# Performance work log

Hardware: AMD Instinct MI355X
Metric: run time of the kernel (lower is better)

The kernel has to match this reference:

```python
import jax, jax.numpy as jnp
import numpy as np

D_MODEL = 1024
N_HEADS = 16
D_HEAD = D_MODEL // N_HEADS


def setup_inputs() -> dict:
    key = jax.random.key(0)
    ks = jax.random.split(key, 11)
    B, S = 2, 2048
    s_in = 1.0 / np.sqrt(D_MODEL)
    return {
        "query": jax.random.normal(ks[0], (B, S, D_MODEL), jnp.float32),
        "key": jax.random.normal(ks[1], (B, S, D_MODEL), jnp.float32),
        "value": jax.random.normal(ks[2], (B, S, D_MODEL), jnp.float32),
        "Wq_w": jax.random.normal(ks[3], (D_MODEL, D_MODEL), jnp.float32) * s_in,
        "Wq_b": jax.random.normal(ks[4], (D_MODEL,), jnp.float32) * 0.01,
        "Wk_w": jax.random.normal(ks[5], (D_HEAD, D_MODEL), jnp.float32) * s_in,
        "Wk_b": jax.random.normal(ks[6], (D_HEAD,), jnp.float32) * 0.01,
        "Wv_w": jax.random.normal(ks[7], (D_HEAD, D_MODEL), jnp.float32) * s_in,
        "Wv_b": jax.random.normal(ks[8], (D_HEAD,), jnp.float32) * 0.01,
        "Wo_w": jax.random.normal(ks[9], (D_MODEL, D_MODEL), jnp.float32) * s_in,
        "Wo_b": jax.random.normal(ks[10], (D_MODEL,), jnp.float32) * 0.01,
    }


def reference(query, key, value, Wq_w, Wq_b, Wk_w, Wk_b, Wv_w, Wv_b, Wo_w, Wo_b):
    B, S, _ = query.shape
    # Q: per-head projection [B, H, S, dh]; K/V: single shared head [B, S, dh]
    Q = (query @ Wq_w.T + Wq_b).reshape(B, S, N_HEADS, D_HEAD).transpose(0, 2, 1, 3)
    K = key @ Wk_w.T + Wk_b      # [B, S, dh], shared across heads (MQA)
    V = value @ Wv_w.T + Wv_b    # [B, S, dh]
    scale = 1.0 / np.sqrt(D_HEAD).astype(np.float32)
    scores = jnp.einsum('bhqd,bkd->bhqk', Q, K) * scale  # [B, H, S, S]
    attn = jax.nn.softmax(scores, axis=-1)
    ctx = jnp.einsum('bhqk,bkd->bhqd', attn, V)           # [B, H, S, dh]
    ctx = ctx.transpose(0, 2, 1, 3).reshape(B, S, D_MODEL)
    out = ctx @ Wo_w.T + Wo_b
    return out, attn
```

## Files before the change

### kernel.cpp

```cpp
#include <hip/hip_runtime.h>
#include <hip/hip_bf16.h>
#include <math.h>

#define D_MODEL 1024
#define N_HEADS 16
#define D_HEAD 64
#define S_ 2048

typedef __attribute__((ext_vector_type(8))) short short8;
typedef __attribute__((ext_vector_type(4))) float f32x4;
typedef __attribute__((ext_vector_type(16))) float f32x16;

static __device__ inline short f2bf(float f) {
    union { __hip_bfloat16 h; short s; } u;
    u.h = __float2bfloat16(f);
    return u.s;
}

static __device__ inline f32x4 mfma16(short8 a, short8 b, f32x4 c) {
    return __builtin_amdgcn_mfma_f32_16x16x32_bf16(a, b, c, 0, 0, 0);
}
static __device__ inline f32x16 mfma32(short8 a, short8 b, f32x16 c) {
    return __builtin_amdgcn_mfma_f32_32x32x16_bf16(a, b, c, 0, 0, 0);
}
static __device__ inline f32x16 zero16() {
    f32x16 z;
#pragma unroll
    for (int i = 0; i < 16; i++) z[i] = 0.f;
    return z;
}

static __device__ inline void load_lds16(const void* g, void* l) {
    __builtin_amdgcn_global_load_lds(
        (const __attribute__((address_space(1))) unsigned int*)g,
        (__attribute__((address_space(3))) unsigned int*)l, 16, 0, 0);
}

__global__ __launch_bounds__(256)
void cvt_all(const float* __restrict__ q, const float* __restrict__ k,
             const float* __restrict__ v, const float* __restrict__ wq,
             const float* __restrict__ wk, const float* __restrict__ wv,
             const float* __restrict__ wo,
             short* dq, short* dk, short* dv, short* dwq, short* dwk,
             short* dwv, short* dwo) {
    size_t c = (size_t)blockIdx.x * 256 + threadIdx.x;
    const float* s; short* d; size_t off;
    if (c < 524288)        { s = q;  d = dq;  off = c; }
    else if (c < 1048576)  { s = k;  d = dk;  off = c - 524288; }
    else if (c < 1572864)  { s = v;  d = dv;  off = c - 1048576; }
    else if (c < 1703936)  { s = wq; d = dwq; off = c - 1572864; }
    else if (c < 1712128)  { s = wk; d = dwk; off = c - 1703936; }
    else if (c < 1720320)  { s = wv; d = dwv; off = c - 1712128; }
    else                   { s = wo; d = dwo; off = c - 1720320; }
    const f32x4* sp = (const f32x4*)(s + off * 8);
    f32x4 a = sp[0], b = sp[1];
    short8 o;
    o[0] = f2bf(a[0]); o[1] = f2bf(a[1]); o[2] = f2bf(a[2]); o[3] = f2bf(a[3]);
    o[4] = f2bf(b[0]); o[5] = f2bf(b[1]); o[6] = f2bf(b[2]); o[7] = f2bf(b[3]);
    *(short8*)(d + off * 8) = o;
}

template<int BM, int BN, int OUT_MODE>
__device__ __forceinline__ void gemm_body(
    const short* __restrict__ A, const short* __restrict__ Wb,
    const float* __restrict__ bias, void* __restrict__ Cv,
    int bx, int by, int M, int N, int K, float out_scale, char* lds)
{
    constexpr int NI = BM / 32, NJ = BN / 32;
    constexpr int AISS = BM / 32, WISS = BN / 32;
    char* As = lds;
    char* Ws = lds + 2 * BM * 128;
    const int t = threadIdx.x, lane = t & 63, w = t >> 6;
    const int wr = w >> 1, wc = w & 1, r15 = lane & 15, g = lane >> 4;
    const int m0 = by * BM, n0 = bx * BN;
    const size_t Kb2 = (size_t)K * 2;

    int aR[AISS > WISS ? AISS : WISS], aC[AISS > WISS ? AISS : WISS];
#pragma unroll
    for (int i = 0; i < (AISS > WISS ? AISS : WISS); i++) {
        int l = i * 4096 + t * 16;
        aR[i] = l >> 7;
        aC[i] = (l & 127) ^ (((l >> 7) & 7) << 4);
    }

    f32x4 acc[NI][NJ];
#pragma unroll
    for (int i = 0; i < NI; i++)
#pragma unroll
        for (int j = 0; j < NJ; j++) acc[i][j] = (f32x4){0.f, 0.f, 0.f, 0.f};

    const int nk = K / 64;
    auto stage = [&](int kt, int buf) {
        size_t kb = (size_t)kt * 128;
#pragma unroll
        for (int i = 0; i < AISS; i++)
            load_lds16((const char*)A + (size_t)(m0 + aR[i]) * Kb2 + kb + aC[i],
                       As + buf * (BM * 128) + i * 4096 + (w << 10));
#pragma unroll
        for (int i = 0; i < WISS; i++)
            load_lds16((const char*)Wb + (size_t)(n0 + aR[i]) * Kb2 + kb + aC[i],
                       Ws + buf * (BN * 128) + i * 4096 + (w << 10));
    };

    stage(0, 0);
    __syncthreads();
    int cur = 0;
    for (int kt = 0; kt < nk; kt++) {
        if (kt + 1 < nk) stage(kt + 1, cur ^ 1);
        const char* Ab = As + cur * (BM * 128);
        const char* Wbs = Ws + cur * (BN * 128);
#pragma unroll
        for (int kc = 0; kc < 2; kc++) {
            short8 af[NI], bw[NJ];
#pragma unroll
            for (int i = 0; i < NI; i++) {
                int r = wr * (16 * NI) + i * 16 + r15;
                af[i] = *(const short8*)(Ab + r * 128 + ((kc * 64 + g * 16) ^ ((r & 7) << 4)));
            }
#pragma unroll
            for (int j = 0; j < NJ; j++) {
                int r = wc * (16 * NJ) + j * 16 + r15;
                bw[j] = *(const short8*)(Wbs + r * 128 + ((kc * 64 + g * 16) ^ ((r & 7) << 4)));
            }
#pragma unroll
            for (int i = 0; i < NI; i++)
#pragma unroll
                for (int j = 0; j < NJ; j++)
                    acc[i][j] = mfma16(af[i], bw[j], acc[i][j]);
        }
        __syncthreads();
        cur ^= 1;
    }

#pragma unroll
    for (int i = 0; i < NI; i++) {
#pragma unroll
        for (int j = 0; j < NJ; j++) {
            int ncol = n0 + wc * (16 * NJ) + j * 16 + r15;
            float bv = bias[ncol];
#pragma unroll
            for (int reg = 0; reg < 4; reg++) {
                int mrow = m0 + wr * (16 * NI) + i * 16 + g * 4 + reg;
                float val = (acc[i][j][reg] + bv) * out_scale;
                if (OUT_MODE == 0) {
                    __builtin_nontemporal_store(val, (float*)Cv + (size_t)mrow * N + ncol);
                } else if (OUT_MODE == 1) {
                    ((short*)Cv)[(size_t)mrow * N + ncol] = f2bf(val);
                } else {
                    ((short*)Cv)[((((size_t)(mrow >> 11)) * 64 + ncol) << 11) +
                                 (mrow & 2047)] = f2bf(val);
                }
            }
        }
    }
}

__global__ __launch_bounds__(256)
void qkv_proj(const short* __restrict__ qin, const short* __restrict__ kin,
              const short* __restrict__ vin, const short* __restrict__ wqb,
              const short* __restrict__ wkb, const short* __restrict__ wvb,
              const float* __restrict__ bq, const float* __restrict__ bk,
              const float* __restrict__ bv,
              short* Qb, short* Kb, short* Vtb) {
    __shared__ char lds[49152];
    int bid = blockIdx.x;
    if (bid < 512)
        gemm_body<64, 128, 1>(qin, wqb, bq, Qb, bid & 7, bid >> 3,
                              4096, 1024, 1024, 0.18033688011112f, lds);
    else if (bid < 576)
        gemm_body<64, 64, 1>(kin, wkb, bk, Kb, 0, bid - 512,
                             4096, 64, 1024, 1.0f, lds);
    else
        gemm_body<64, 64, 2>(vin, wvb, bv, Vtb, 0, bid - 576,
                             4096, 64, 1024, 1.0f, lds);
}

__global__ __launch_bounds__(256)
void o_proj(const short* __restrict__ ctxb, const short* __restrict__ wob,
            const float* __restrict__ bo, float* __restrict__ out) {
    __shared__ char lds[49152];
    gemm_body<64, 128, 0>(ctxb, wob, bo, out, blockIdx.x & 7, blockIdx.x >> 3,
                          4096, 1024, 1024, 1.0f, lds);
}

__global__ __launch_bounds__(128)
void mqa_attn5(const short* __restrict__ Qb,
               const short* __restrict__ Kb,
               const short* __restrict__ Vtb,
               float* __restrict__ attn,
               short* __restrict__ ctxb)
{
    __shared__ short KB2[2][4096];
    __shared__ short VB2[2][4096];
    __shared__ short Ps[4096];

    const int t = threadIdx.x, lane = t & 63, w = t >> 6;
    const int l31 = lane & 31, h5 = lane >> 5;
    const int bid = blockIdx.x;
    const int qt = bid & 31, h = (bid >> 5) & 15, b = bid >> 9;
    const int q0 = qt * 64;
    const int wq = w * 32;

    short8 aq[4];
    {
        const char* qbase = (const char*)(Qb +
            (size_t)(b * S_ + q0 + wq + l31) * D_MODEL + h * 64);
#pragma unroll
        for (int kc = 0; kc < 4; kc++)
            aq[kc] = *(const short8*)(qbase + kc * 32 + h5 * 16);
    }

    int koA[4], vcR[4];
    const char* vrowp[4];
#pragma unroll
    for (int i = 0; i < 4; i++) {
        int l = i * 2048 + t * 16;
        int row = l >> 7;
        koA[i] = l ^ ((row & 7) << 4);
        int vc = (l & 127) ^ ((row & 7) << 4);
        vrowp[i] = (const char*)(Vtb + (((size_t)(b * 64 + row)) << 11)) + vc;
    }
    const char* ktile0 = (const char*)(Kb + (size_t)b * S_ * 64);

#define STAGE_K(kti, buf) {                                                    \
        const char* kb_ = ktile0 + (size_t)(kti) * 8192;                       \
        load_lds16(kb_ + koA[0], (char*)KB2 + (buf) * 8192 + 0 * 2048 + (w << 10)); \
        load_lds16(kb_ + koA[1], (char*)KB2 + (buf) * 8192 + 1 * 2048 + (w << 10)); \
        load_lds16(kb_ + koA[2], (char*)KB2 + (buf) * 8192 + 2 * 2048 + (w << 10)); \
        load_lds16(kb_ + koA[3], (char*)KB2 + (buf) * 8192 + 3 * 2048 + (w << 10)); }
#define STAGE_V(kti, buf) {                                                    \
        load_lds16(vrowp[0] + (size_t)(kti) * 128, (char*)VB2 + (buf) * 8192 + 0 * 2048 + (w << 10)); \
        load_lds16(vrowp[1] + (size_t)(kti) * 128, (char*)VB2 + (buf) * 8192 + 1 * 2048 + (w << 10)); \
        load_lds16(vrowp[2] + (size_t)(kti) * 128, (char*)VB2 + (buf) * 8192 + 2 * 2048 + (w << 10)); \
        load_lds16(vrowp[3] + (size_t)(kti) * 128, (char*)VB2 + (buf) * 8192 + 3 * 2048 + (w << 10)); }
#define RD(base, r, cb) (*(const short8*)((const char*)(base) + (r) * 128 + ((cb) ^ (((r) & 7) << 4))))

    float lsum[16];
#pragma unroll
    for (int reg = 0; reg < 16; reg++) lsum[reg] = 0.f;

    int cur = 0;
    STAGE_K(0, 0);
    __syncthreads();
    for (int kti = 0; kti < 32; kti++) {
        if (kti + 1 < 32) STAGE_K(kti + 1, cur ^ 1);
        f32x16 s0 = zero16(), s1 = zero16();
#pragma unroll
        for (int kc = 0; kc < 4; kc++) {
            s0 = mfma32(aq[kc], RD(KB2[cur], l31, kc * 32 + h5 * 16), s0);
            s1 = mfma32(aq[kc], RD(KB2[cur], 32 + l31, kc * 32 + h5 * 16), s1);
        }
#pragma unroll
        for (int reg = 0; reg < 16; reg++)
            lsum[reg] += exp2f(s0[reg]) + exp2f(s1[reg]);
        __syncthreads();
        cur ^= 1;
    }

    float inv[16];
#pragma unroll
    for (int reg = 0; reg < 16; reg++) {
        float v = lsum[reg];
        v += __shfl_xor(v, 1); v += __shfl_xor(v, 2);
        v += __shfl_xor(v, 4); v += __shfl_xor(v, 8); v += __shfl_xor(v, 16);
        inv[reg] = 1.f / v;
    }

    f32x16 ctxA = zero16(), ctxB = zero16();
    float* attn_base = attn +
        (((size_t)((b * 16 + h) * 2048 + q0 + wq + 4 * h5)) << 11) + l31;

    cur = 0;
    STAGE_K(0, 0);
    STAGE_V(0, 0);
    __syncthreads();
    for (int kti = 0; kti < 32; kti++) {
        if (kti + 1 < 32) { STAGE_K(kti + 1, cur ^ 1); STAGE_V(kti + 1, cur ^ 1); }
        f32x16 s0 = zero16(), s1 = zero16();
#pragma unroll
        for (int kc = 0; kc < 4; kc++) {
            s0 = mfma32(aq[kc], RD(KB2[cur], l31, kc * 32 + h5 * 16), s0);
            s1 = mfma32(aq[kc], RD(KB2[cur], 32 + l31, kc * 32 + h5 * 16), s1);
        }
        float* arowptr = attn_base + (size_t)kti * 64;
#pragma unroll
        for (int reg = 0; reg < 16; reg++) {
            const int rloc = (reg & 3) + 8 * (reg >> 2);
            const int rps = wq + rloc + 4 * h5;
            float p0 = exp2f(s0[reg]) * inv[reg];
            __builtin_nontemporal_store(p0, arowptr + ((size_t)rloc << 11));
            *(short*)((char*)Ps + rps * 128 + ((l31 * 2) ^ ((rps & 7) << 4))) = f2bf(p0);
            float p1 = exp2f(s1[reg]) * inv[reg];
            __builtin_nontemporal_store(p1, arowptr + ((size_t)rloc << 11) + 32);
            *(short*)((char*)Ps + rps * 128 + ((64 + l31 * 2) ^ ((rps & 7) << 4))) = f2bf(p1);
        }
        short8 ap[4];
#pragma unroll
        for (int kc = 0; kc < 4; kc++)
            ap[kc] = RD(Ps, wq + l31, kc * 32 + h5 * 16);
#pragma unroll
        for (int kc = 0; kc < 4; kc++) {
            ctxA = mfma32(ap[kc], RD(VB2[cur], l31, kc * 32 + h5 * 16), ctxA);
            ctxB = mfma32(ap[kc], RD(VB2[cur], 32 + l31, kc * 32 + h5 * 16), ctxB);
        }
        __syncthreads();
        cur ^= 1;
    }

    const int tokbase = b * 2048 + q0 + wq + 4 * h5;
#pragma unroll
    for (int reg = 0; reg < 16; reg++) {
        const int rloc = (reg & 3) + 8 * (reg >> 2);
        size_t base = (size_t)(tokbase + rloc) * D_MODEL + h * 64 + l31;
        ctxb[base]      = f2bf(ctxA[reg]);
        ctxb[base + 32] = f2bf(ctxB[reg]);
    }
#undef STAGE_K
#undef STAGE_V
#undef RD
}

extern "C" void kernel_launch(void* const* d_in, const int* in_sizes, int n_in,
                              void* d_out, int out_size, void* d_ws, size_t ws_size,
                              hipStream_t stream) {
    const float* query = (const float*)d_in[0];
    const float* key   = (const float*)d_in[1];
    const float* value = (const float*)d_in[2];
    const float* Wq_w  = (const float*)d_in[3];
    const float* Wq_b  = (const float*)d_in[4];
    const float* Wk_w  = (const float*)d_in[5];
    const float* Wk_b  = (const float*)d_in[6];
    const float* Wv_w  = (const float*)d_in[7];
    const float* Wv_b  = (const float*)d_in[8];
    const float* Wo_w  = (const float*)d_in[9];
    const float* Wo_b  = (const float*)d_in[10];

    short* ws   = (short*)d_ws;
    short* qin  = ws;
    short* kin  = qin  + (size_t)4194304;
    short* vin  = kin  + (size_t)4194304;
    short* wqb  = vin  + (size_t)4194304;
    short* wkb  = wqb  + (size_t)1048576;
    short* wvb  = wkb  + (size_t)65536;
    short* wob  = wvb  + (size_t)65536;
    short* Qb   = wob  + (size_t)1048576;
    short* Kb   = Qb   + (size_t)4194304;
    short* Vtb  = Kb   + (size_t)262144;
    short* ctxb = Vtb  + (size_t)262144;

    float* out  = (float*)d_out;
    float* attn = out + (size_t)4096 * 1024;

    dim3 blk(256);

    cvt_all<<<dim3(7232), blk, 0, stream>>>(query, key, value, Wq_w, Wk_w, Wv_w,
                                            Wo_w, qin, kin, vin, wqb, wkb, wvb, wob);
    qkv_proj<<<dim3(640), blk, 0, stream>>>(qin, kin, vin, wqb, wkb, wvb,
                                            Wq_b, Wk_b, Wv_b, Qb, Kb, Vtb);
    mqa_attn5<<<dim3(1024), dim3(128), 0, stream>>>(Qb, Kb, Vtb, attn, ctxb);
    o_proj<<<dim3(512), blk, 0, stream>>>(ctxb, wob, Wo_b, out);
}
```

Baseline: 217.8 us.

## Fold softmax normalization into MFMA accumulator, pack P stores, add setprio

The attention pass now seeds the score accumulator with -log2(rowsum), so exp2 yields normalized probabilities directly and the per-element multiply goes away. P is written to LDS as packed bf16 pairs through v_cvt_pk_bf16_f32, which needs the V^T columns permuted in the projection epilogue so the packed P layout still matches the V tile. MFMA sections are wrapped in s_setprio to favour matrix issue across waves. The permuted Vt layout and the log-domain normalization add coupling between kernels and may change rounding slightly.

```diff
diff --git a/kernel.cpp b/kernel.cpp
--- a/kernel.cpp
+++ b/kernel.cpp
@@ -15,6 +15,12 @@
     union { __hip_bfloat16 h; short s; } u;
     u.h = __float2bfloat16(f);
     return u.s;
+}
+
+static __device__ inline unsigned pk_bf16(float a, float b) {
+    unsigned r;
+    asm("v_cvt_pk_bf16_f32 %0, %1, %2" : "=v"(r) : "v"(a), "v"(b));
+    return r;
 }
 
 static __device__ inline f32x4 mfma16(short8 a, short8 b, f32x4 c) {
@@ -147,8 +153,10 @@
                 } else if (OUT_MODE == 1) {
                     ((short*)Cv)[(size_t)mrow * N + ncol] = f2bf(val);
                 } else {
-                    ((short*)Cv)[((((size_t)(mrow >> 11)) * 64 + ncol) << 11) +
-                                 (mrow & 2047)] = f2bf(val);
+                    int sb = mrow & 2047;
+                    int scol = (sb & ~63) | ((sb & 31) << 1) | ((sb & 32) >> 5);
+                    ((short*)Cv)[((((size_t)(mrow >> 11)) * 64 + ncol) << 11) + scol] =
+                        f2bf(val);
                 }
             }
         }
@@ -184,7 +192,7 @@
 }
 
 __global__ __launch_bounds__(128)
-void mqa_attn5(const short* __restrict__ Qb,
+void mqa_attn6(const short* __restrict__ Qb,
                const short* __restrict__ Kb,
                const short* __restrict__ Vtb,
                float* __restrict__ attn,
@@ -210,7 +218,7 @@
             aq[kc] = *(const short8*)(qbase + kc * 32 + h5 * 16);
     }
 
-    int koA[4], vcR[4];
+    int koA[4];
     const char* vrowp[4];
 #pragma unroll
     for (int i = 0; i < 4; i++) {
@@ -245,11 +253,13 @@
     for (int kti = 0; kti < 32; kti++) {
         if (kti + 1 < 32) STAGE_K(kti + 1, cur ^ 1);
         f32x16 s0 = zero16(), s1 = zero16();
+        __builtin_amdgcn_s_setprio(1);
 #pragma unroll
         for (int kc = 0; kc < 4; kc++) {
             s0 = mfma32(aq[kc], RD(KB2[cur], l31, kc * 32 + h5 * 16), s0);
             s1 = mfma32(aq[kc], RD(KB2[cur], 32 + l31, kc * 32 + h5 * 16), s1);
         }
+        __builtin_amdgcn_s_setprio(0);
 #pragma unroll
         for (int reg = 0; reg < 16; reg++)
             lsum[reg] += exp2f(s0[reg]) + exp2f(s1[reg]);
@@ -257,13 +267,13 @@
         cur ^= 1;
     }
 
-    float inv[16];
+    float c_[16];
 #pragma unroll
     for (int reg = 0; reg < 16; reg++) {
         float v = lsum[reg];
         v += __shfl_xor(v, 1); v += __shfl_xor(v, 2);
         v += __shfl_xor(v, 4); v += __shfl_xor(v, 8); v += __shfl_xor(v, 16);
-        inv[reg] = 1.f / v;
+        c_[reg] = -log2f(v);
     }
 
     f32x16 ctxA = zero16(), ctxB = zero16();
@@ -276,33 +286,39 @@
     __syncthreads();
     for (int kti = 0; kti < 32; kti++) {
         if (kti + 1 < 32) { STAGE_K(kti + 1, cur ^ 1); STAGE_V(kti + 1, cur ^ 1); }
-        f32x16 s0 = zero16(), s1 = zero16();
+        f32x16 s0, s1;
+#pragma unroll
+        for (int reg = 0; reg < 16; reg++) { s0[reg] = c_[reg]; s1[reg] = c_[reg]; }
+        __builtin_amdgcn_s_setprio(1);
 #pragma unroll
         for (int kc = 0; kc < 4; kc++) {
             s0 = mfma32(aq[kc], RD(KB2[cur], l31, kc * 32 + h5 * 16), s0);
             s1 = mfma32(aq[kc], RD(KB2[cur], 32 + l31, kc * 32 + h5 * 16), s1);
         }
+        __builtin_amdgcn_s_setprio(0);
         float* arowptr = attn_base + (size_t)kti * 64;
 #pragma unroll
         for (int reg = 0; reg < 16; reg++) {
             const int rloc = (reg & 3) + 8 * (reg >> 2);
             const int rps = wq + rloc + 4 * h5;
-            float p0 = exp2f(s0[reg]) * inv[reg];
+            float p0 = exp2f(s0[reg]);
+            float p1 = exp2f(s1[reg]);
             __builtin_nontemporal_store(p0, arowptr + ((size_t)rloc << 11));
-            *(short*)((char*)Ps + rps * 128 + ((l31 * 2) ^ ((rps & 7) << 4))) = f2bf(p0);
-            float p1 = exp2f(s1[reg]) * inv[reg];
             __builtin_nontemporal_store(p1, arowptr + ((size_t)rloc << 11) + 32);
-            *(short*)((char*)Ps + rps * 128 + ((64 + l31 * 2) ^ ((rps & 7) << 4))) = f2bf(p1);
+            *(unsigned*)((char*)Ps + rps * 128 + ((4 * l31) ^ ((rps & 7) << 4))) =
+                pk_bf16(p0, p1);
         }
         short8 ap[4];
 #pragma unroll
         for (int kc = 0; kc < 4; kc++)
             ap[kc] = RD(Ps, wq + l31, kc * 32 + h5 * 16);
+        __builtin_amdgcn_s_setprio(1);
 #pragma unroll
         for (int kc = 0; kc < 4; kc++) {
             ctxA = mfma32(ap[kc], RD(VB2[cur], l31, kc * 32 + h5 * 16), ctxA);
             ctxB = mfma32(ap[kc], RD(VB2[cur], 32 + l31, kc * 32 + h5 * 16), ctxB);
         }
+        __builtin_amdgcn_s_setprio(0);
         __syncthreads();
         cur ^= 1;
     }
@@ -357,6 +373,6 @@
                                             Wo_w, qin, kin, vin, wqb, wkb, wvb, wob);
     qkv_proj<<<dim3(640), blk, 0, stream>>>(qin, kin, vin, wqb, wkb, wvb,
                                             Wq_b, Wk_b, Wv_b, Qb, Kb, Vtb);
-    mqa_attn5<<<dim3(1024), dim3(128), 0, stream>>>(Qb, Kb, Vtb, attn, ctxb);
+    mqa_attn6<<<dim3(1024), dim3(128), 0, stream>>>(Qb, Kb, Vtb, attn, ctxb);
     o_proj<<<dim3(512), blk, 0, stream>>>(ctxb, wob, Wo_b, out);
 }
```

After: 221.5 us. No clear change (+1.7%).

## Process two query tiles per block, fusing second tile's row-sum pass into first tile's output pass

Applied to the files above, without the earlier changes.

Each attention block now handles 128 query rows as two 64-row halves instead of one. The row-sum (first) pass for the second half is folded into the output pass of the first half, so the K tiles loaded there serve both halves. This cuts total K/V staging passes per 128 rows from four to three, removing redundant K loads and QK MFMAs. In exchange the grid is halved to 512 blocks, which lowers parallelism and occupancy, and register pressure rises from the extra Q fragments and accumulators.

```diff
diff --git a/kernel.cpp b/kernel.cpp
--- a/kernel.cpp
+++ b/kernel.cpp
@@ -184,11 +184,11 @@
 }
 
 __global__ __launch_bounds__(128)
-void mqa_attn5(const short* __restrict__ Qb,
-               const short* __restrict__ Kb,
-               const short* __restrict__ Vtb,
-               float* __restrict__ attn,
-               short* __restrict__ ctxb)
+void mqa_attn10(const short* __restrict__ Qb,
+                const short* __restrict__ Kb,
+                const short* __restrict__ Vtb,
+                float* __restrict__ attn,
+                short* __restrict__ ctxb)
 {
     __shared__ short KB2[2][4096];
     __shared__ short VB2[2][4096];
@@ -197,20 +197,23 @@
     const int t = threadIdx.x, lane = t & 63, w = t >> 6;
     const int l31 = lane & 31, h5 = lane >> 5;
     const int bid = blockIdx.x;
-    const int qt = bid & 31, h = (bid >> 5) & 15, b = bid >> 9;
-    const int q0 = qt * 64;
+    const int qt2 = bid & 15, h = (bid >> 4) & 15, b = bid >> 8;
+    const int q0 = qt2 * 128;
     const int wq = w * 32;
 
-    short8 aq[4];
+    short8 aqA[4], aqB[4];
     {
-        const char* qbase = (const char*)(Qb +
+        const char* qbA = (const char*)(Qb +
             (size_t)(b * S_ + q0 + wq + l31) * D_MODEL + h * 64);
-#pragma unroll
-        for (int kc = 0; kc < 4; kc++)
-            aq[kc] = *(const short8*)(qbase + kc * 32 + h5 * 16);
-    }
-
-    int koA[4], vcR[4];
+        const char* qbB = qbA + (size_t)64 * D_MODEL * 2;
+#pragma unroll
+        for (int kc = 0; kc < 4; kc++) {
+            aqA[kc] = *(const short8*)(qbA + kc * 32 + h5 * 16);
+            aqB[kc] = *(const short8*)(qbB + kc * 32 + h5 * 16);
+        }
+    }
+
+    int koA[4];
     const char* vrowp[4];
 #pragma unroll
     for (int i = 0; i < 4; i++) {
@@ -235,9 +238,9 @@
         load_lds16(vrowp[3] + (size_t)(kti) * 128, (char*)VB2 + (buf) * 8192 + 3 * 2048 + (w << 10)); }
 #define RD(base, r, cb) (*(const short8*)((const char*)(base) + (r) * 128 + ((cb) ^ (((r) & 7) << 4))))
 
-    float lsum[16];
-#pragma unroll
-    for (int reg = 0; reg < 16; reg++) lsum[reg] = 0.f;
+    float lsumA[16];
+#pragma unroll
+    for (int reg = 0; reg < 16; reg++) lsumA[reg] = 0.f;
 
     int cur = 0;
     STAGE_K(0, 0);
@@ -247,27 +250,31 @@
         f32x16 s0 = zero16(), s1 = zero16();
 #pragma unroll
         for (int kc = 0; kc < 4; kc++) {
-            s0 = mfma32(aq[kc], RD(KB2[cur], l31, kc * 32 + h5 * 16), s0);
-            s1 = mfma32(aq[kc], RD(KB2[cur], 32 + l31, kc * 32 + h5 * 16), s1);
+            s0 = mfma32(aqA[kc], RD(KB2[cur], l31, kc * 32 + h5 * 16), s0);
+            s1 = mfma32(aqA[kc], RD(KB2[cur], 32 + l31, kc * 32 + h5 * 16), s1);
         }
 #pragma unroll
         for (int reg = 0; reg < 16; reg++)
-            lsum[reg] += exp2f(s0[reg]) + exp2f(s1[reg]);
+            lsumA[reg] += exp2f(s0[reg]) + exp2f(s1[reg]);
         __syncthreads();
         cur ^= 1;
     }
 
-    float inv[16];
+    float invA[16];
 #pragma unroll
     for (int reg = 0; reg < 16; reg++) {
-        float v = lsum[reg];
+        float v = lsumA[reg];
         v += __shfl_xor(v, 1); v += __shfl_xor(v, 2);
         v += __shfl_xor(v, 4); v += __shfl_xor(v, 8); v += __shfl_xor(v, 16);
-        inv[reg] = 1.f / v;
-    }
-
-    f32x16 ctxA = zero16(), ctxB = zero16();
-    float* attn_base = attn +
+        invA[reg] = 1.f / v;
+    }
+
+    f32x16 ctxA0 = zero16(), ctxA1 = zero16();
+    float lsumB[16];
+#pragma unroll
+    for (int reg = 0; reg < 16; reg++) lsumB[reg] = 0.f;
+
+    float* arowA = attn +
         (((size_t)((b * 16 + h) * 2048 + q0 + wq + 4 * h5)) << 11) + l31;
 
     cur = 0;
@@ -279,19 +286,19 @@
         f32x16 s0 = zero16(), s1 = zero16();
 #pragma unroll
         for (int kc = 0; kc < 4; kc++) {
-            s0 = mfma32(aq[kc], RD(KB2[cur], l31, kc * 32 + h5 * 16), s0);
-            s1 = mfma32(aq[kc], RD(KB2[cur], 32 + l31, kc * 32 + h5 * 16), s1);
-        }
-        float* arowptr = attn_base + (size_t)kti * 64;
+            s0 = mfma32(aqA[kc], RD(KB2[cur], l31, kc * 32 + h5 * 16), s0);
+            s1 = mfma32(aqA[kc], RD(KB2[cur], 32 + l31, kc * 32 + h5 * 16), s1);
+        }
+        float* arowptr = arowA + (size_t)kti * 64;
 #pragma unroll
         for (int reg = 0; reg < 16; reg++) {
             const int rloc = (reg & 3) + 8 * (reg >> 2);
             const int rps = wq + rloc + 4 * h5;
-            float p0 = exp2f(s0[reg]) * inv[reg];
+            float p0 = exp2f(s0[reg]) * invA[reg];
+            float p1 = exp2f(s1[reg]) * invA[reg];
             __builtin_nontemporal_store(p0, arowptr + ((size_t)rloc << 11));
+            __builtin_nontemporal_store(p1, arowptr + ((size_t)rloc << 11) + 32);
             *(short*)((char*)Ps + rps * 128 + ((l31 * 2) ^ ((rps & 7) << 4))) = f2bf(p0);
-            float p1 = exp2f(s1[reg]) * inv[reg];
-            __builtin_nontemporal_store(p1, arowptr + ((size_t)rloc << 11) + 32);
             *(short*)((char*)Ps + rps * 128 + ((64 + l31 * 2) ^ ((rps & 7) << 4))) = f2bf(p1);
         }
         short8 ap[4];
@@ -300,20 +307,91 @@
             ap[kc] = RD(Ps, wq + l31, kc * 32 + h5 * 16);
 #pragma unroll
         for (int kc = 0; kc < 4; kc++) {
-            ctxA = mfma32(ap[kc], RD(VB2[cur], l31, kc * 32 + h5 * 16), ctxA);
-            ctxB = mfma32(ap[kc], RD(VB2[cur], 32 + l31, kc * 32 + h5 * 16), ctxB);
-        }
+            ctxA0 = mfma32(ap[kc], RD(VB2[cur], l31, kc * 32 + h5 * 16), ctxA0);
+            ctxA1 = mfma32(ap[kc], RD(VB2[cur], 32 + l31, kc * 32 + h5 * 16), ctxA1);
+        }
+        f32x16 t0 = zero16(), t1 = zero16();
+#pragma unroll
+        for (int kc = 0; kc < 4; kc++) {
+            t0 = mfma32(aqB[kc], RD(KB2[cur], l31, kc * 32 + h5 * 16), t0);
+            t1 = mfma32(aqB[kc], RD(KB2[cur], 32 + l31, kc * 32 + h5 * 16), t1);
+        }
+#pragma unroll
+        for (int reg = 0; reg < 16; reg++)
+            lsumB[reg] += exp2f(t0[reg]) + exp2f(t1[reg]);
         __syncthreads();
         cur ^= 1;
     }
 
-    const int tokbase = b * 2048 + q0 + wq + 4 * h5;
+    {
+        const int tokbase = b * 2048 + q0 + wq + 4 * h5;
+#pragma unroll
+        for (int reg = 0; reg < 16; reg++) {
+            const int rloc = (reg & 3) + 8 * (reg >> 2);
+            size_t base = (size_t)(tokbase + rloc) * D_MODEL + h * 64 + l31;
+            ctxb[base]      = f2bf(ctxA0[reg]);
+            ctxb[base + 32] = f2bf(ctxA1[reg]);
+        }
+    }
+    float invB[16];
 #pragma unroll
     for (int reg = 0; reg < 16; reg++) {
-        const int rloc = (reg & 3) + 8 * (reg >> 2);
-        size_t base = (size_t)(tokbase + rloc) * D_MODEL + h * 64 + l31;
-        ctxb[base]      = f2bf(ctxA[reg]);
-        ctxb[base + 32] = f2bf(ctxB[reg]);
+        float v = lsumB[reg];
+        v += __shfl_xor(v, 1); v += __shfl_xor(v, 2);
+        v += __shfl_xor(v, 4); v += __shfl_xor(v, 8); v += __shfl_xor(v, 16);
+        invB[reg] = 1.f / v;
+    }
+
+    f32x16 ctxB0 = zero16(), ctxB1 = zero16();
+    float* arowB = attn +
+        (((size_t)((b * 16 + h) * 2048 + q0 + 64 + wq + 4 * h5)) << 11) + l31;
+
+    cur = 0;
+    STAGE_K(0, 0);
+    STAGE_V(0, 0);
+    __syncthreads();
+    for (int kti = 0; kti < 32; kti++) {
+        if (kti + 1 < 32) { STAGE_K(kti + 1, cur ^ 1); STAGE_V(kti + 1, cur ^ 1); }
+        f32x16 s0 = zero16(), s1 = zero16();
+#pragma unroll
+        for (int kc = 0; kc < 4; kc++) {
+            s0 = mfma32(aqB[kc], RD(KB2[cur], l31, kc * 32 + h5 * 16), s0);
+            s1 = mfma32(aqB[kc], RD(KB2[cur], 32 + l31, kc * 32 + h5 * 16), s1);
+        }
+        float* arowptr = arowB + (size_t)kti * 64;
+#pragma unroll
+        for (int reg = 0; reg < 16; reg++) {
+            const int rloc = (reg & 3) + 8 * (reg >> 2);
+            const int rps = wq + rloc + 4 * h5;
+            float p0 = exp2f(s0[reg]) * invB[reg];
+            float p1 = exp2f(s1[reg]) * invB[reg];
+            __builtin_nontemporal_store(p0, arowptr + ((size_t)rloc << 11));
+            __builtin_nontemporal_store(p1, arowptr + ((size_t)rloc << 11) + 32);
+            *(short*)((char*)Ps + rps * 128 + ((l31 * 2) ^ ((rps & 7) << 4))) = f2bf(p0);
+            *(short*)((char*)Ps + rps * 128 + ((64 + l31 * 2) ^ ((rps & 7) << 4))) = f2bf(p1);
+        }
+        short8 ap[4];
+#pragma unroll
+        for (int kc = 0; kc < 4; kc++)
+            ap[kc] = RD(Ps, wq + l31, kc * 32 + h5 * 16);
+#pragma unroll
+        for (int kc = 0; kc < 4; kc++) {
+            ctxB0 = mfma32(ap[kc], RD(VB2[cur], l31, kc * 32 + h5 * 16), ctxB0);
+            ctxB1 = mfma32(ap[kc], RD(VB2[cur], 32 + l31, kc * 32 + h5 * 16), ctxB1);
+        }
+        __syncthreads();
+        cur ^= 1;
+    }
+
+    {
+        const int tokbase = b * 2048 + q0 + 64 + wq + 4 * h5;
+#pragma unroll
+        for (int reg = 0; reg < 16; reg++) {
+            const int rloc = (reg & 3) + 8 * (reg >> 2);
+            size_t base = (size_t)(tokbase + rloc) * D_MODEL + h * 64 + l31;
+            ctxb[base]      = f2bf(ctxB0[reg]);
+            ctxb[base + 32] = f2bf(ctxB1[reg]);
+        }
     }
 #undef STAGE_K
 #undef STAGE_V
@@ -357,6 +435,6 @@
                                             Wo_w, qin, kin, vin, wqb, wkb, wvb, wob);
     qkv_proj<<<dim3(640), blk, 0, stream>>>(qin, kin, vin, wqb, wkb, wvb,
                                             Wq_b, Wk_b, Wv_b, Qb, Kb, Vtb);
-    mqa_attn5<<<dim3(1024), dim3(128), 0, stream>>>(Qb, Kb, Vtb, attn, ctxb);
+    mqa_attn10<<<dim3(512), dim3(128), 0, stream>>>(Qb, Kb, Vtb, attn, ctxb);
     o_proj<<<dim3(512), blk, 0, stream>>>(ctxb, wob, Wo_b, out);
 }
```

Result: slower. 245.9 us (+12.9%).

## Split attention key dimension across waves with 32-row query tiles

Applied to the files above, without the earlier changes.

The attention kernel now gives each block 32 query rows instead of 64 and launches twice as many blocks. Within a block, the two waves split each 64-key tile, each computing a 32x32 score block, instead of each wave owning its own 32 query rows. Row sums and partial context outputs are combined across waves through LDS, which adds extra barriers and a final reduction. The intent is more parallelism and less per-wave register pressure, at the cost of each block re-staging K/V for fewer query rows, which doubles total K/V staging traffic.

```diff
diff --git a/kernel.cpp b/kernel.cpp
--- a/kernel.cpp
+++ b/kernel.cpp
@@ -184,33 +184,32 @@
 }
 
 __global__ __launch_bounds__(128)
-void mqa_attn5(const short* __restrict__ Qb,
-               const short* __restrict__ Kb,
-               const short* __restrict__ Vtb,
-               float* __restrict__ attn,
-               short* __restrict__ ctxb)
+void mqa_attn11(const short* __restrict__ Qb,
+                const short* __restrict__ Kb,
+                const short* __restrict__ Vtb,
+                float* __restrict__ attn,
+                short* __restrict__ ctxb)
 {
     __shared__ short KB2[2][4096];
     __shared__ short VB2[2][4096];
-    __shared__ short Ps[4096];
+    __shared__ short Ps[2048];
 
     const int t = threadIdx.x, lane = t & 63, w = t >> 6;
     const int l31 = lane & 31, h5 = lane >> 5;
     const int bid = blockIdx.x;
-    const int qt = bid & 31, h = (bid >> 5) & 15, b = bid >> 9;
-    const int q0 = qt * 64;
-    const int wq = w * 32;
+    const int qt = bid & 63, h = (bid >> 6) & 15, b = bid >> 10;
+    const int q0 = qt * 32;
 
     short8 aq[4];
     {
         const char* qbase = (const char*)(Qb +
-            (size_t)(b * S_ + q0 + wq + l31) * D_MODEL + h * 64);
+            (size_t)(b * S_ + q0 + l31) * D_MODEL + h * 64);
 #pragma unroll
         for (int kc = 0; kc < 4; kc++)
             aq[kc] = *(const short8*)(qbase + kc * 32 + h5 * 16);
     }
 
-    int koA[4], vcR[4];
+    int koA[4];
     const char* vrowp[4];
 #pragma unroll
     for (int i = 0; i < 4; i++) {
@@ -244,31 +243,39 @@
     __syncthreads();
     for (int kti = 0; kti < 32; kti++) {
         if (kti + 1 < 32) STAGE_K(kti + 1, cur ^ 1);
-        f32x16 s0 = zero16(), s1 = zero16();
-#pragma unroll
-        for (int kc = 0; kc < 4; kc++) {
-            s0 = mfma32(aq[kc], RD(KB2[cur], l31, kc * 32 + h5 * 16), s0);
-            s1 = mfma32(aq[kc], RD(KB2[cur], 32 + l31, kc * 32 + h5 * 16), s1);
-        }
-#pragma unroll
-        for (int reg = 0; reg < 16; reg++)
-            lsum[reg] += exp2f(s0[reg]) + exp2f(s1[reg]);
+        f32x16 s = zero16();
+#pragma unroll
+        for (int kc = 0; kc < 4; kc++)
+            s = mfma32(aq[kc], RD(KB2[cur], 32 * w + l31, kc * 32 + h5 * 16), s);
+#pragma unroll
+        for (int reg = 0; reg < 16; reg++) lsum[reg] += exp2f(s[reg]);
         __syncthreads();
         cur ^= 1;
     }
 
     float inv[16];
-#pragma unroll
-    for (int reg = 0; reg < 16; reg++) {
-        float v = lsum[reg];
-        v += __shfl_xor(v, 1); v += __shfl_xor(v, 2);
-        v += __shfl_xor(v, 4); v += __shfl_xor(v, 8); v += __shfl_xor(v, 16);
-        inv[reg] = 1.f / v;
+    {
+        float* psred = (float*)Ps;
+#pragma unroll
+        for (int reg = 0; reg < 16; reg++) {
+            float v = lsum[reg];
+            v += __shfl_xor(v, 1); v += __shfl_xor(v, 2);
+            v += __shfl_xor(v, 4); v += __shfl_xor(v, 8); v += __shfl_xor(v, 16);
+            if (l31 == 0)
+                psred[w * 32 + (reg & 3) + 8 * (reg >> 2) + 4 * h5] = v;
+        }
+        __syncthreads();
+#pragma unroll
+        for (int reg = 0; reg < 16; reg++) {
+            int r = (reg & 3) + 8 * (reg >> 2) + 4 * h5;
+            inv[reg] = 1.f / (psred[r] + psred[32 + r]);
+        }
+        __syncthreads();
     }
 
     f32x16 ctxA = zero16(), ctxB = zero16();
-    float* attn_base = attn +
-        (((size_t)((b * 16 + h) * 2048 + q0 + wq + 4 * h5)) << 11) + l31;
+    float* arow = attn +
+        (((size_t)((b * 16 + h) * 2048 + q0 + 4 * h5)) << 11) + 32 * w + l31;
 
     cur = 0;
     STAGE_K(0, 0);
@@ -276,44 +283,53 @@
     __syncthreads();
     for (int kti = 0; kti < 32; kti++) {
         if (kti + 1 < 32) { STAGE_K(kti + 1, cur ^ 1); STAGE_V(kti + 1, cur ^ 1); }
-        f32x16 s0 = zero16(), s1 = zero16();
-#pragma unroll
-        for (int kc = 0; kc < 4; kc++) {
-            s0 = mfma32(aq[kc], RD(KB2[cur], l31, kc * 32 + h5 * 16), s0);
-            s1 = mfma32(aq[kc], RD(KB2[cur], 32 + l31, kc * 32 + h5 * 16), s1);
-        }
-        float* arowptr = attn_base + (size_t)kti * 64;
+        f32x16 s = zero16();
+#pragma unroll
+        for (int kc = 0; kc < 4; kc++)
+            s = mfma32(aq[kc], RD(KB2[cur], 32 * w + l31, kc * 32 + h5 * 16), s);
+        float* aptr = arow + (size_t)kti * 64;
 #pragma unroll
         for (int reg = 0; reg < 16; reg++) {
             const int rloc = (reg & 3) + 8 * (reg >> 2);
-            const int rps = wq + rloc + 4 * h5;
-            float p0 = exp2f(s0[reg]) * inv[reg];
-            __builtin_nontemporal_store(p0, arowptr + ((size_t)rloc << 11));
-            *(short*)((char*)Ps + rps * 128 + ((l31 * 2) ^ ((rps & 7) << 4))) = f2bf(p0);
-            float p1 = exp2f(s1[reg]) * inv[reg];
-            __builtin_nontemporal_store(p1, arowptr + ((size_t)rloc << 11) + 32);
-            *(short*)((char*)Ps + rps * 128 + ((64 + l31 * 2) ^ ((rps & 7) << 4))) = f2bf(p1);
-        }
-        short8 ap[4];
-#pragma unroll
-        for (int kc = 0; kc < 4; kc++)
-            ap[kc] = RD(Ps, wq + l31, kc * 32 + h5 * 16);
-#pragma unroll
-        for (int kc = 0; kc < 4; kc++) {
-            ctxA = mfma32(ap[kc], RD(VB2[cur], l31, kc * 32 + h5 * 16), ctxA);
-            ctxB = mfma32(ap[kc], RD(VB2[cur], 32 + l31, kc * 32 + h5 * 16), ctxB);
+            const int rps = rloc + 4 * h5;
+            float p = exp2f(s[reg]) * inv[reg];
+            __builtin_nontemporal_store(p, aptr + ((size_t)rloc << 11));
+            *(short*)((char*)Ps + rps * 128 +
+                      ((64 * w + l31 * 2) ^ ((rps & 7) << 4))) = f2bf(p);
+        }
+        short8 ap[2];
+#pragma unroll
+        for (int j = 0; j < 2; j++)
+            ap[j] = RD(Ps, l31, (2 * w + j) * 32 + h5 * 16);
+#pragma unroll
+        for (int j = 0; j < 2; j++) {
+            ctxA = mfma32(ap[j], RD(VB2[cur], l31, (2 * w + j) * 32 + h5 * 16), ctxA);
+            ctxB = mfma32(ap[j], RD(VB2[cur], 32 + l31, (2 * w + j) * 32 + h5 * 16), ctxB);
         }
         __syncthreads();
         cur ^= 1;
     }
 
-    const int tokbase = b * 2048 + q0 + wq + 4 * h5;
-#pragma unroll
-    for (int reg = 0; reg < 16; reg++) {
-        const int rloc = (reg & 3) + 8 * (reg >> 2);
-        size_t base = (size_t)(tokbase + rloc) * D_MODEL + h * 64 + l31;
-        ctxb[base]      = f2bf(ctxA[reg]);
-        ctxb[base + 32] = f2bf(ctxB[reg]);
+    float* red = (float*)KB2;
+    if (w == 1) {
+#pragma unroll
+        for (int reg = 0; reg < 16; reg++) {
+            int r = (reg & 3) + 8 * (reg >> 2) + 4 * h5;
+            red[r * 64 + l31]      = ctxA[reg];
+            red[r * 64 + 32 + l31] = ctxB[reg];
+        }
+    }
+    __syncthreads();
+    if (w == 0) {
+        const int tokbase = b * 2048 + q0 + 4 * h5;
+#pragma unroll
+        for (int reg = 0; reg < 16; reg++) {
+            const int rloc = (reg & 3) + 8 * (reg >> 2);
+            int r = rloc + 4 * h5;
+            size_t base = (size_t)(tokbase + rloc) * D_MODEL + h * 64 + l31;
+            ctxb[base]      = f2bf(ctxA[reg] + red[r * 64 + l31]);
+            ctxb[base + 32] = f2bf(ctxB[reg] + red[r * 64 + 32 + l31]);
+        }
     }
 #undef STAGE_K
 #undef STAGE_V
@@ -357,6 +373,6 @@
                                             Wo_w, qin, kin, vin, wqb, wkb, wvb, wob);
     qkv_proj<<<dim3(640), blk, 0, stream>>>(qin, kin, vin, wqb, wkb, wvb,
                                             Wq_b, Wk_b, Wv_b, Qb, Kb, Vtb);
-    mqa_attn5<<<dim3(1024), dim3(128), 0, stream>>>(Qb, Kb, Vtb, attn, ctxb);
+    mqa_attn11<<<dim3(2048), dim3(128), 0, stream>>>(Qb, Kb, Vtb, attn, ctxb);
     o_proj<<<dim3(512), blk, 0, stream>>>(ctxb, wob, Wo_b, out);
 }
```

Result: slower. 281.1 us (+29.1%).
